# Optimization experiments

Hardware: AMD Instinct MI355X
Metric: run time of the kernel (lower is better)

## Reference

```python
import jax, jax.numpy as jnp
import numpy as np

EMBED_DIM = 1024
NUM_HEADS = 16
HEAD_DIM = EMBED_DIM // NUM_HEADS


def setup_inputs() -> dict:
    key = jax.random.key(0)
    k_x, k_wqkv, k_bqkv, k_wout, k_bout = jax.random.split(key, 5)
    B, T, C = 2, 2048, EMBED_DIM
    s = 1.0 / np.sqrt(C)
    return {
        "x": jax.random.normal(k_x, (B, T, C), dtype=jnp.float32),
        "W_qkv": jax.random.uniform(k_wqkv, (C, 3 * C), jnp.float32, -s, s),
        "b_qkv": jax.random.uniform(k_bqkv, (3 * C,), jnp.float32, -s, s),
        "W_out": jax.random.uniform(k_wout, (C, C), jnp.float32, -s, s),
        "b_out": jax.random.uniform(k_bout, (C,), jnp.float32, -s, s),
    }


def reference(x, W_qkv, b_qkv, W_out, b_out):
    B, T, C = x.shape
    H, D = NUM_HEADS, HEAD_DIM
    qkv = x @ W_qkv + b_qkv                      # [B,T,3C]
    # Faithful to torch: reshape to [B,T,H,3D], move heads, chunk last dim.
    qkv = qkv.reshape(B, T, H, 3 * D).transpose(0, 2, 1, 3)  # [B,H,T,3D]
    q, k, v = qkv[..., :D], qkv[..., D:2 * D], qkv[..., 2 * D:]
    scores = jnp.einsum("bhqd,bhkd->bhqk", q, k) / np.sqrt(D).astype(jnp.float32)
    weights = jax.nn.softmax(scores, axis=-1)    # [B,H,T,T]
    attn = jnp.einsum("bhqk,bhkd->bhqd", weights, v)  # [B,H,T,D]
    attn = attn.transpose(0, 2, 1, 3).reshape(B, T, C)
    return attn @ W_out + b_out
```

## Files before the change

### kernel.cpp

```cpp
#include <hip/hip_runtime.h>


typedef float  f32x4  __attribute__((ext_vector_type(4)));
typedef __bf16 bf16x8 __attribute__((ext_vector_type(8)));

#define QSCALE 0.18033688011112042f

#if __has_builtin(__builtin_amdgcn_exp2f)
#define EXP2(x) __builtin_amdgcn_exp2f(x)
#else
#define EXP2(x) exp2f(x)
#endif
#if __has_builtin(__builtin_amdgcn_rcpf)
#define RCP(x) __builtin_amdgcn_rcpf(x)
#else
#define RCP(x) (1.0f / (x))
#endif

static __device__ __forceinline__ f32x4 mfma32(bf16x8 a, bf16x8 b, f32x4 c) {
    return __builtin_amdgcn_mfma_f32_16x16x32_bf16(a, b, c, 0, 0, 0);
}

static __device__ __forceinline__ bf16x8 ld8(const unsigned short* p) {
    return __builtin_bit_cast(bf16x8, *(const uint4*)p);
}
static __device__ __forceinline__ unsigned short bfbits(float f) {
    __bf16 h = (__bf16)f;
    return __builtin_bit_cast(unsigned short, h);
}

static __device__ __forceinline__ void glds16(const unsigned short* g,
                                              unsigned short* lds_base) {
    __builtin_amdgcn_global_load_lds(
        (const __attribute__((address_space(1))) unsigned int*)g,
        (__attribute__((address_space(3))) unsigned int*)lds_base, 16, 0, 0);
}

__global__ __launch_bounds__(256) void prep_kernel(
    const float* __restrict__ x, unsigned short* __restrict__ xb,
    const float* __restrict__ Wqkv, unsigned short* __restrict__ wqkvT,
    const float* __restrict__ Wout, unsigned short* __restrict__ woutT) {
    __shared__ float tile[32][33];
    const int bid = blockIdx.x;
    if (bid < 4096) {
        int i = bid * 256 + threadIdx.x;
        float4 v = ((const float4*)x)[i];
        ushort4 o;
        o.x = bfbits(v.x); o.y = bfbits(v.y);
        o.z = bfbits(v.z); o.w = bfbits(v.w);
        ((ushort4*)xb)[i] = o;
        return;
    }
    const float* W; unsigned short* Wt; int N, n0, k0;
    if (bid < 7168) {
        int l = bid - 4096; W = Wqkv; Wt = wqkvT; N = 3072;
        n0 = (l % 96) * 32; k0 = (l / 96) * 32;
    } else {
        int l = bid - 7168; W = Wout; Wt = woutT; N = 1024;
        n0 = (l & 31) * 32; k0 = (l >> 5) * 32;
    }
    int tx = threadIdx.x & 31, ty = threadIdx.x >> 5;
#pragma unroll
    for (int i = 0; i < 4; i++) {
        int r = ty + i * 8;
        tile[r][tx] = W[(size_t)(k0 + r) * N + n0 + tx];
    }
    __syncthreads();
#pragma unroll
    for (int i = 0; i < 4; i++) {
        int r = ty + i * 8;
        Wt[(size_t)(n0 + r) * 1024 + k0 + tx] = bfbits(tile[tx][r]);
    }
}

__global__ __launch_bounds__(256) void qkv_gemm_kernel(
    const unsigned short* __restrict__ A, const unsigned short* __restrict__ Bt,
    const float* __restrict__ bias, unsigned short* __restrict__ Qb,
    unsigned short* __restrict__ Kb, unsigned short* __restrict__ Vtb) {
    __shared__ unsigned short As[2][128 * 32];
    __shared__ unsigned short Bs[2][128 * 32];
    const int wg = blockIdx.x;
    const int xcd = wg & 7, local = wg >> 3;
    const int n_t = (xcd >> 2) * 12 + local % 12;
    const int m_t = (xcd & 3) * 8 + local / 12;
    const int m0 = m_t * 128, n0 = n_t * 128;
    const int tid = threadIdx.x;
    const int lane = tid & 63, w = tid >> 6;
    const int ln = lane & 15, quad = lane >> 4;
    const int wm = (w >> 1) * 64, wn = (w & 1) * 64;
    const int sr = lane >> 2, sc = (lane & 3) * 8;
    f32x4 acc[4][4] = {};
#pragma unroll
    for (int i = 0; i < 2; i++) {
        int r0 = w * 32 + i * 16;
        glds16(&A[(size_t)(m0 + r0 + sr) * 1024 + sc], &As[0][r0 * 32]);
        glds16(&Bt[(size_t)(n0 + r0 + sr) * 1024 + sc], &Bs[0][r0 * 32]);
    }
    __syncthreads();
    for (int kt = 0; kt < 32; kt++) {
        const int cur = kt & 1;
        if (kt + 1 < 32) {
            const int nxt = cur ^ 1;
            const int kc = (kt + 1) * 32;
#pragma unroll
            for (int i = 0; i < 2; i++) {
                int r0 = w * 32 + i * 16;
                glds16(&A[(size_t)(m0 + r0 + sr) * 1024 + kc + sc], &As[nxt][r0 * 32]);
                glds16(&Bt[(size_t)(n0 + r0 + sr) * 1024 + kc + sc], &Bs[nxt][r0 * 32]);
            }
        }
        bf16x8 af[4], bf[4];
#pragma unroll
        for (int mi = 0; mi < 4; mi++)
            af[mi] = ld8(&As[cur][(wm + mi * 16 + ln) * 32 + quad * 8]);
#pragma unroll
        for (int ni = 0; ni < 4; ni++)
            bf[ni] = ld8(&Bs[cur][(wn + ni * 16 + ln) * 32 + quad * 8]);
#pragma unroll
        for (int mi = 0; mi < 4; mi++)
#pragma unroll
            for (int ni = 0; ni < 4; ni++)
                acc[mi][ni] = mfma32(af[mi], bf[ni], acc[mi][ni]);
        __syncthreads();
    }
#pragma unroll
    for (int mi = 0; mi < 4; mi++)
#pragma unroll
        for (int ni = 0; ni < 4; ni++) {
            int gn = n0 + wn + ni * 16 + ln;
            float bi = bias[gn];
            int h = gn / 192, rr = gn - h * 192;
            int gm0 = m0 + wm + mi * 16 + quad * 4;
            int b = gm0 >> 11, t0 = gm0 & 2047;
            float vv[4];
#pragma unroll
            for (int r = 0; r < 4; r++) vv[r] = acc[mi][ni][r] + bi;
            if (rr < 64) {
                size_t base = ((size_t)(b * 16 + h) * 2048 + t0) * 64 + rr;
#pragma unroll
                for (int r = 0; r < 4; r++)
                    Qb[base + (size_t)r * 64] = bfbits(vv[r] * QSCALE);
            } else if (rr < 128) {
                size_t base = ((size_t)(b * 16 + h) * 2048 + t0) * 64 + rr - 64;
#pragma unroll
                for (int r = 0; r < 4; r++)
                    Kb[base + (size_t)r * 64] = bfbits(vv[r]);
            } else {
                int tp0 = (t0 & ~31) | (quad << 3) | ((mi & 1) << 2);
                ushort4 pk;
                pk.x = bfbits(vv[0]); pk.y = bfbits(vv[1]);
                pk.z = bfbits(vv[2]); pk.w = bfbits(vv[3]);
                *(ushort4*)&Vtb[((size_t)(b * 16 + h) * 64 + (rr - 128)) * 2048
                                + tp0] = pk;
            }
        }
}

__global__ __launch_bounds__(512)
__attribute__((amdgpu_waves_per_eu(4, 4)))
void attn_kernel(
    const unsigned short* __restrict__ Q, const unsigned short* __restrict__ K,
    const unsigned short* __restrict__ Vt, unsigned short* __restrict__ Ob) {
    __shared__ unsigned short smem[2][2][2][4096];
    const int wg  = blockIdx.x;
    const int xcd = wg & 7, local = wg >> 3;
    const int bh  = xcd * 4 + (local >> 4);
    const int qt  = local & 15;
    const int tid = threadIdx.x;
    const int lane = tid & 63, w = tid >> 6;
    const int w4 = w & 3, ks = w >> 2;
    const int ln = lane & 15, quad = lane >> 4;
    const int lr = lane >> 3, lg = lane & 7;
    const int e = ln & 7;

    unsigned short (*Ks)[4096] = smem[ks][0];
    unsigned short (*Vs)[4096] = smem[ks][1];

    const unsigned short* Qg = Q + ((size_t)bh * 2048 + qt * 128) * 64;
    const unsigned short* Kg = K + ((size_t)bh * 2048 + ks * 1024) * 64;
    const unsigned short* Vg = Vt + (size_t)bh * 64 * 2048 + ks * 1024;

    bf16x8 qf[2][2];
#pragma unroll
    for (int h = 0; h < 2; h++) {
        const unsigned short* qp = Qg + (size_t)(w4 * 32 + h * 16 + ln) * 64;
        qf[h][0] = ld8(qp + quad * 8);
        qf[h][1] = ld8(qp + 32 + quad * 8);
    }

    const unsigned short* kb0 = &Ks[0][ln * 64 + (quad ^ e) * 8];
    const unsigned short* kb1 = &Ks[0][ln * 64 + ((4 + quad) ^ e) * 8];
    const unsigned short* vp0 = &Vs[0][ln * 64 + (quad ^ e) * 8];
    const unsigned short* vp1 = &Vs[0][ln * 64 + ((4 + quad) ^ e) * 8];

    const int kof0 = (w4 * 16 + lr) * 64 + (lg ^ lr) * 8;
    const int kof1 = (w4 * 16 + 8 + lr) * 64 + (lg ^ lr) * 8;
    const int vof0 = (w4 * 16 + lr) * 2048 + (lg ^ lr) * 8;
    const int vof1 = (w4 * 16 + 8 + lr) * 2048 + (lg ^ lr) * 8;
    unsigned short* kd0[2] = {&Ks[0][(w4 * 16) * 64], &Ks[1][(w4 * 16) * 64]};
    unsigned short* kd1[2] = {&Ks[0][(w4 * 16 + 8) * 64], &Ks[1][(w4 * 16 + 8) * 64]};
    unsigned short* vd0[2] = {&Vs[0][(w4 * 16) * 64], &Vs[1][(w4 * 16) * 64]};
    unsigned short* vd1[2] = {&Vs[0][(w4 * 16 + 8) * 64], &Vs[1][(w4 * 16 + 8) * 64]};

    glds16(Kg + kof0, kd0[0]);
    glds16(Kg + kof1, kd1[0]);
    glds16(Vg + vof0, vd0[0]);
    glds16(Vg + vof1, vd1[0]);
    __syncthreads();

    const unsigned short* KgR = Kg + 4096;
    const unsigned short* VgR = Vg + 64;

    bf16x8 ones8;
#pragma unroll
    for (int j = 0; j < 8; j++) ones8[j] = __bf16(1.0f);
    f32x4 zero4 = {};
    asm volatile("" : "+v"(zero4));
    f32x4 o[2][4] = {};
    f32x4 lacc[2] = {};

#define ATTN_TILE(CUR, PREF)                                                  \
    do {                                                                      \
        if (PREF) {                                                           \
            glds16(KgR + kof0, kd0[CUR ^ 1]);                                 \
            glds16(KgR + kof1, kd1[CUR ^ 1]);                                 \
            glds16(VgR + vof0, vd0[CUR ^ 1]);                                 \
            glds16(VgR + vof1, vd1[CUR ^ 1]);                                 \
            KgR += 4096; VgR += 64;                                           \
        }                                                                     \
        f32x4 s[2][4];                                                        \
        __builtin_amdgcn_s_setprio(1);                                        \
        _Pragma("unroll")                                                     \
        for (int ms = 0; ms < 4; ms++) {                                      \
            bf16x8 a0 = ld8(kb0 + (CUR) * 4096 + ms * 1024);                  \
            bf16x8 a1 = ld8(kb1 + (CUR) * 4096 + ms * 1024);                  \
            _Pragma("unroll")                                                 \
            for (int h = 0; h < 2; h++) {                                     \
                s[h][ms] = mfma32(a0, qf[h][0], zero4);                       \
                s[h][ms] = mfma32(a1, qf[h][1], s[h][ms]);                    \
            }                                                                 \
        }                                                                     \
        __builtin_amdgcn_s_setprio(0);                                        \
        bf16x8 pb8[2][2];                                                     \
        _Pragma("unroll")                                                     \
        for (int h = 0; h < 2; h++)                                           \
            _Pragma("unroll")                                                 \
            for (int p = 0; p < 2; p++) {                                     \
                f32x4 e0, e1;                                                 \
                e0[0] = EXP2(s[h][2 * p][0]); e0[1] = EXP2(s[h][2 * p][1]);   \
                e0[2] = EXP2(s[h][2 * p][2]); e0[3] = EXP2(s[h][2 * p][3]);   \
                e1[0] = EXP2(s[h][2 * p + 1][0]);                             \
                e1[1] = EXP2(s[h][2 * p + 1][1]);                             \
                e1[2] = EXP2(s[h][2 * p + 1][2]);                             \
                e1[3] = EXP2(s[h][2 * p + 1][3]);                             \
                pb8[h][p][0] = __bf16(e0[0]); pb8[h][p][1] = __bf16(e0[1]);   \
                pb8[h][p][2] = __bf16(e0[2]); pb8[h][p][3] = __bf16(e0[3]);   \
                pb8[h][p][4] = __bf16(e1[0]); pb8[h][p][5] = __bf16(e1[1]);   \
                pb8[h][p][6] = __bf16(e1[2]); pb8[h][p][7] = __bf16(e1[3]);   \
            }                                                                 \
        __builtin_amdgcn_s_setprio(1);                                        \
        _Pragma("unroll")                                                     \
        for (int h = 0; h < 2; h++)                                           \
            _Pragma("unroll")                                                 \
            for (int p = 0; p < 2; p++)                                       \
                lacc[h] = mfma32(ones8, pb8[h][p], lacc[h]);                  \
        _Pragma("unroll")                                                     \
        for (int df = 0; df < 4; df++) {                                      \
            bf16x8 a80 = ld8(vp0 + (CUR) * 4096 + df * 1024);                 \
            o[0][df] = mfma32(a80, pb8[0][0], o[0][df]);                      \
            o[1][df] = mfma32(a80, pb8[1][0], o[1][df]);                      \
            bf16x8 a81 = ld8(vp1 + (CUR) * 4096 + df * 1024);                 \
            o[0][df] = mfma32(a81, pb8[0][1], o[0][df]);                      \
            o[1][df] = mfma32(a81, pb8[1][1], o[1][df]);                      \
        }                                                                     \
        __builtin_amdgcn_s_setprio(0);                                        \
        __syncthreads();                                                      \
    } while (0)

    for (int it = 0; it < 8; it++) {
        ATTN_TILE(0, true);
        ATTN_TILE(1, (it < 7));
    }
#undef ATTN_TILE

    float* xf = (float*)&smem[0][0][0][0];
    const int slot = w4 * 64 + lane;
    if (ks) {
#pragma unroll
        for (int h = 0; h < 2; h++)
#pragma unroll
            for (int df = 0; df < 4; df++) {
                int j = h * 4 + df;
                *(f32x4*)(xf + (size_t)(slot * 8 + (j ^ (slot & 7))) * 4) = o[h][df];
            }
        xf[8192 + slot * 2 + 0] = lacc[0][0];
        xf[8192 + slot * 2 + 1] = lacc[1][0];
    }
    __syncthreads();
    if (!ks) {
        float inv0 = RCP(lacc[0][0] + xf[8192 + slot * 2 + 0]);
        float inv1 = RCP(lacc[1][0] + xf[8192 + slot * 2 + 1]);
        const int b = bh >> 4, hh = bh & 15;
#pragma unroll
        for (int h = 0; h < 2; h++) {
            float inv = h ? inv1 : inv0;
            int qrow = qt * 128 + w4 * 32 + h * 16 + ln;
            size_t row = ((size_t)b * 2048 + qrow) * 1024 + hh * 64;
#pragma unroll
            for (int df = 0; df < 4; df++) {
                int j = h * 4 + df;
                f32x4 oo = *(const f32x4*)(xf + (size_t)(slot * 8 + (j ^ (slot & 7))) * 4);
                ushort4 pk;
                pk.x = bfbits((o[h][df][0] + oo[0]) * inv);
                pk.y = bfbits((o[h][df][1] + oo[1]) * inv);
                pk.z = bfbits((o[h][df][2] + oo[2]) * inv);
                pk.w = bfbits((o[h][df][3] + oo[3]) * inv);
                *(ushort4*)&Ob[row + df * 16 + quad * 4] = pk;
            }
        }
    }
}

__global__ __launch_bounds__(256) void out_gemm_kernel(
    const unsigned short* __restrict__ A, const unsigned short* __restrict__ Bt,
    const float* __restrict__ bias, float* __restrict__ out) {
    __shared__ unsigned short As[2][64 * 32];
    __shared__ unsigned short Bs[2][128 * 32];
    const int wg = blockIdx.x;
    const int xcd = wg & 7, local = wg >> 3;
    const int m_t = xcd * 8 + (local & 7);
    const int n_t = local >> 3;
    const int m0 = m_t * 64, n0 = n_t * 128;
    const int tid = threadIdx.x;
    const int lane = tid & 63, w = tid >> 6;
    const int ln = lane & 15, quad = lane >> 4;
    const int wm = (w >> 1) * 32, wn = (w & 1) * 64;
    const int sr = lane >> 2, sc = (lane & 3) * 8;
    f32x4 acc[2][4] = {};
    {
        int ra = w * 16;
        glds16(&A[(size_t)(m0 + ra + sr) * 1024 + sc], &As[0][ra * 32]);
#pragma unroll
        for (int i = 0; i < 2; i++) {
            int rb = w * 32 + i * 16;
            glds16(&Bt[(size_t)(n0 + rb + sr) * 1024 + sc], &Bs[0][rb * 32]);
        }
    }
    __syncthreads();
    for (int kt = 0; kt < 32; kt++) {
        const int cur = kt & 1;
        if (kt + 1 < 32) {
            const int nxt = cur ^ 1;
            const int kc = (kt + 1) * 32;
            int ra = w * 16;
            glds16(&A[(size_t)(m0 + ra + sr) * 1024 + kc + sc], &As[nxt][ra * 32]);
#pragma unroll
            for (int i = 0; i < 2; i++) {
                int rb = w * 32 + i * 16;
                glds16(&Bt[(size_t)(n0 + rb + sr) * 1024 + kc + sc], &Bs[nxt][rb * 32]);
            }
        }
        bf16x8 af[2], bf[4];
#pragma unroll
        for (int mi = 0; mi < 2; mi++)
            af[mi] = ld8(&As[cur][(wm + mi * 16 + ln) * 32 + quad * 8]);
#pragma unroll
        for (int ni = 0; ni < 4; ni++)
            bf[ni] = ld8(&Bs[cur][(wn + ni * 16 + ln) * 32 + quad * 8]);
#pragma unroll
        for (int mi = 0; mi < 2; mi++)
#pragma unroll
            for (int ni = 0; ni < 4; ni++)
                acc[mi][ni] = mfma32(af[mi], bf[ni], acc[mi][ni]);
        __syncthreads();
    }
#pragma unroll
    for (int mi = 0; mi < 2; mi++)
#pragma unroll
        for (int ni = 0; ni < 4; ni++) {
            int gn = n0 + wn + ni * 16 + ln;
            float bi = bias[gn];
#pragma unroll
            for (int r = 0; r < 4; r++) {
                int gm = m0 + wm + mi * 16 + quad * 4 + r;
                out[(size_t)gm * 1024 + gn] = acc[mi][ni][r] + bi;
            }
        }
}

extern "C" void kernel_launch(void* const* d_in, const int* in_sizes, int n_in,
                              void* d_out, int out_size, void* d_ws, size_t ws_size,
                              hipStream_t stream) {
    const float* x     = (const float*)d_in[0];
    const float* W_qkv = (const float*)d_in[1];
    const float* b_qkv = (const float*)d_in[2];
    const float* W_out = (const float*)d_in[3];
    const float* b_out = (const float*)d_in[4];
    float* out = (float*)d_out;

    char* ws = (char*)d_ws;
    unsigned short* xb    = (unsigned short*)(ws);
    unsigned short* wqkvT = (unsigned short*)(ws + (size_t)( 8 << 20));
    unsigned short* woutT = (unsigned short*)(ws + (size_t)(14 << 20));
    unsigned short* Qb    = (unsigned short*)(ws + (size_t)(16 << 20));
    unsigned short* Kb    = (unsigned short*)(ws + (size_t)(24 << 20));
    unsigned short* Vtb   = (unsigned short*)(ws + (size_t)(32 << 20));
    unsigned short* attnb = (unsigned short*)(ws + (size_t)(40 << 20));

    prep_kernel<<<8192, 256, 0, stream>>>(x, xb, W_qkv, wqkvT, W_out, woutT);
    qkv_gemm_kernel<<<768, 256, 0, stream>>>(xb, wqkvT, b_qkv, Qb, Kb, Vtb);
    attn_kernel<<<512, 512, 0, stream>>>(Qb, Kb, Vtb, attnb);
    out_gemm_kernel<<<512, 256, 0, stream>>>(attnb, woutT, b_out, out);
}
```

Measured before the change: 177.0 us.

## Enlarge QKV GEMM tiles to 256x192 with 512 threads aligned to heads

The QKV projection GEMM goes from 128x128 tiles with 256 threads to 256x192 tiles with 512 threads (8 waves, each computing 64x96). Each N tile now matches one head's 192-column q/k/v slice, so the head index is simply the tile index and the per-element division is gone. The aim is more data reuse per LDS load and fewer workgroups (256 instead of 768), with the XCD mapping adjusted to match. The cost is more LDS and registers per block and only 256 blocks, which may under-fill the GPU's compute units.

```diff
diff --git a/kernel.cpp b/kernel.cpp
--- a/kernel.cpp
+++ b/kernel.cpp
@@ -73,63 +73,67 @@
     }
 }
 
-__global__ __launch_bounds__(256) void qkv_gemm_kernel(
+__global__ __launch_bounds__(512) void qkv_gemm_kernel(
     const unsigned short* __restrict__ A, const unsigned short* __restrict__ Bt,
     const float* __restrict__ bias, unsigned short* __restrict__ Qb,
     unsigned short* __restrict__ Kb, unsigned short* __restrict__ Vtb) {
-    __shared__ unsigned short As[2][128 * 32];
-    __shared__ unsigned short Bs[2][128 * 32];
+    __shared__ unsigned short As[2][256 * 32];
+    __shared__ unsigned short Bs[2][192 * 32];
     const int wg = blockIdx.x;
     const int xcd = wg & 7, local = wg >> 3;
-    const int n_t = (xcd >> 2) * 12 + local % 12;
-    const int m_t = (xcd & 3) * 8 + local / 12;
-    const int m0 = m_t * 128, n0 = n_t * 128;
+    const int n_t = (xcd & 3) * 4 + (local & 3);
+    const int m_t = (xcd >> 2) * 8 + (local >> 2);
+    const int m0 = m_t * 256, n0 = n_t * 192;
     const int tid = threadIdx.x;
     const int lane = tid & 63, w = tid >> 6;
     const int ln = lane & 15, quad = lane >> 4;
-    const int wm = (w >> 1) * 64, wn = (w & 1) * 64;
+    const int wm = (w >> 1) * 64;
+    const int wn = (w & 1) * 96;
     const int sr = lane >> 2, sc = (lane & 3) * 8;
-    f32x4 acc[4][4] = {};
-#pragma unroll
-    for (int i = 0; i < 2; i++) {
-        int r0 = w * 32 + i * 16;
-        glds16(&A[(size_t)(m0 + r0 + sr) * 1024 + sc], &As[0][r0 * 32]);
-        glds16(&Bt[(size_t)(n0 + r0 + sr) * 1024 + sc], &Bs[0][r0 * 32]);
-    }
+
+    f32x4 acc[4][6] = {};
+
+#define STAGE(BUF, KC)                                                        \
+    do {                                                                      \
+        glds16(&A[(size_t)(m0 + w * 16 + sr) * 1024 + (KC) + sc],             \
+               &As[BUF][(w * 16) * 32]);                                      \
+        glds16(&A[(size_t)(m0 + 128 + w * 16 + sr) * 1024 + (KC) + sc],       \
+               &As[BUF][(128 + w * 16) * 32]);                                \
+        glds16(&Bt[(size_t)(n0 + w * 16 + sr) * 1024 + (KC) + sc],            \
+               &Bs[BUF][(w * 16) * 32]);                                      \
+        if (w < 4)                                                            \
+            glds16(&Bt[(size_t)(n0 + 128 + w * 16 + sr) * 1024 + (KC) + sc],  \
+                   &Bs[BUF][(128 + w * 16) * 32]);                            \
+    } while (0)
+
+    STAGE(0, 0);
     __syncthreads();
     for (int kt = 0; kt < 32; kt++) {
         const int cur = kt & 1;
-        if (kt + 1 < 32) {
-            const int nxt = cur ^ 1;
-            const int kc = (kt + 1) * 32;
-#pragma unroll
-            for (int i = 0; i < 2; i++) {
-                int r0 = w * 32 + i * 16;
-                glds16(&A[(size_t)(m0 + r0 + sr) * 1024 + kc + sc], &As[nxt][r0 * 32]);
-                glds16(&Bt[(size_t)(n0 + r0 + sr) * 1024 + kc + sc], &Bs[nxt][r0 * 32]);
-            }
-        }
-        bf16x8 af[4], bf[4];
+        if (kt + 1 < 32) STAGE(cur ^ 1, (kt + 1) * 32);
+        bf16x8 af[4], bf[6];
 #pragma unroll
         for (int mi = 0; mi < 4; mi++)
             af[mi] = ld8(&As[cur][(wm + mi * 16 + ln) * 32 + quad * 8]);
 #pragma unroll
-        for (int ni = 0; ni < 4; ni++)
+        for (int ni = 0; ni < 6; ni++)
             bf[ni] = ld8(&Bs[cur][(wn + ni * 16 + ln) * 32 + quad * 8]);
 #pragma unroll
         for (int mi = 0; mi < 4; mi++)
 #pragma unroll
-            for (int ni = 0; ni < 4; ni++)
+            for (int ni = 0; ni < 6; ni++)
                 acc[mi][ni] = mfma32(af[mi], bf[ni], acc[mi][ni]);
         __syncthreads();
     }
+#undef STAGE
+
+    const int h = n_t;
 #pragma unroll
     for (int mi = 0; mi < 4; mi++)
 #pragma unroll
-        for (int ni = 0; ni < 4; ni++) {
-            int gn = n0 + wn + ni * 16 + ln;
-            float bi = bias[gn];
-            int h = gn / 192, rr = gn - h * 192;
+        for (int ni = 0; ni < 6; ni++) {
+            int rr = wn + ni * 16 + ln;
+            float bi = bias[n0 + rr];
             int gm0 = m0 + wm + mi * 16 + quad * 4;
             int b = gm0 >> 11, t0 = gm0 & 2047;
             float vv[4];
@@ -408,7 +412,7 @@
     unsigned short* attnb = (unsigned short*)(ws + (size_t)(40 << 20));
 
     prep_kernel<<<8192, 256, 0, stream>>>(x, xb, W_qkv, wqkvT, W_out, woutT);
-    qkv_gemm_kernel<<<768, 256, 0, stream>>>(xb, wqkvT, b_qkv, Qb, Kb, Vtb);
+    qkv_gemm_kernel<<<256, 512, 0, stream>>>(xb, wqkvT, b_qkv, Qb, Kb, Vtb);
     attn_kernel<<<512, 512, 0, stream>>>(Qb, Kb, Vtb, attnb);
     out_gemm_kernel<<<512, 256, 0, stream>>>(attnb, woutT, b_out, out);
 }
```

New measurement: 173.9 us. Within noise of the previous version (-1.8%).

## Triple-buffer QKV GEMM LDS staging with one barrier per k-step

Applied to the files above, without the earlier changes.

The QKV projection GEMM goes from double to triple-buffered LDS tiles. Global-to-LDS loads are issued two k-steps ahead, and the waits use explicit vmcnt counts with a single s_barrier per iteration instead of a full __syncthreads after compute. Address pointers are precomputed, and the MFMA block is wrapped in s_setprio to favour matrix issue. This aims to hide global load latency and cut barrier stalls, at the cost of extra LDS per block, which may reduce occupancy.

```diff
diff --git a/kernel.cpp b/kernel.cpp
--- a/kernel.cpp
+++ b/kernel.cpp
@@ -77,8 +77,8 @@
     const unsigned short* __restrict__ A, const unsigned short* __restrict__ Bt,
     const float* __restrict__ bias, unsigned short* __restrict__ Qb,
     unsigned short* __restrict__ Kb, unsigned short* __restrict__ Vtb) {
-    __shared__ unsigned short As[2][128 * 32];
-    __shared__ unsigned short Bs[2][128 * 32];
+    __shared__ unsigned short As[3][128 * 32];
+    __shared__ unsigned short Bs[3][128 * 32];
     const int wg = blockIdx.x;
     const int xcd = wg & 7, local = wg >> 3;
     const int n_t = (xcd >> 2) * 12 + local % 12;
@@ -89,40 +89,67 @@
     const int ln = lane & 15, quad = lane >> 4;
     const int wm = (w >> 1) * 64, wn = (w & 1) * 64;
     const int sr = lane >> 2, sc = (lane & 3) * 8;
+
+    const unsigned short* a_rd = &As[0][(wm + ln) * 32 + quad * 8];
+    const unsigned short* b_rd = &Bs[0][(wn + ln) * 32 + quad * 8];
+    unsigned short* a_st0 = &As[0][(w * 32) * 32];
+    unsigned short* a_st1 = &As[0][(w * 32 + 16) * 32];
+    unsigned short* b_st0 = &Bs[0][(w * 32) * 32];
+    unsigned short* b_st1 = &Bs[0][(w * 32 + 16) * 32];
+    const unsigned short* Ag0 = &A[(size_t)(m0 + w * 32 + sr) * 1024 + sc];
+    const unsigned short* Ag1 = &A[(size_t)(m0 + w * 32 + 16 + sr) * 1024 + sc];
+    const unsigned short* Bg0 = &Bt[(size_t)(n0 + w * 32 + sr) * 1024 + sc];
+    const unsigned short* Bg1 = &Bt[(size_t)(n0 + w * 32 + 16 + sr) * 1024 + sc];
+
+#define QSTAGE(OFF, KC)                                                       \
+    do {                                                                      \
+        glds16(Ag0 + (KC), a_st0 + (OFF));                                    \
+        glds16(Bg0 + (KC), b_st0 + (OFF));                                    \
+        glds16(Ag1 + (KC), a_st1 + (OFF));                                    \
+        glds16(Bg1 + (KC), b_st1 + (OFF));                                    \
+    } while (0)
+
+#define QCOMPUTE(CO)                                                          \
+    do {                                                                      \
+        bf16x8 af[4], bf[4];                                                  \
+        _Pragma("unroll")                                                     \
+        for (int mi = 0; mi < 4; mi++)                                        \
+            af[mi] = ld8(a_rd + (CO) + mi * 512);                             \
+        _Pragma("unroll")                                                     \
+        for (int ni = 0; ni < 4; ni++)                                        \
+            bf[ni] = ld8(b_rd + (CO) + ni * 512);                             \
+        __builtin_amdgcn_s_setprio(1);                                        \
+        _Pragma("unroll")                                                     \
+        for (int mi = 0; mi < 4; mi++)                                        \
+            _Pragma("unroll")                                                 \
+            for (int ni = 0; ni < 4; ni++)                                    \
+                acc[mi][ni] = mfma32(af[mi], bf[ni], acc[mi][ni]);            \
+        __builtin_amdgcn_s_setprio(0);                                        \
+    } while (0)
+
     f32x4 acc[4][4] = {};
-#pragma unroll
-    for (int i = 0; i < 2; i++) {
-        int r0 = w * 32 + i * 16;
-        glds16(&A[(size_t)(m0 + r0 + sr) * 1024 + sc], &As[0][r0 * 32]);
-        glds16(&Bt[(size_t)(n0 + r0 + sr) * 1024 + sc], &Bs[0][r0 * 32]);
-    }
-    __syncthreads();
-    for (int kt = 0; kt < 32; kt++) {
-        const int cur = kt & 1;
-        if (kt + 1 < 32) {
-            const int nxt = cur ^ 1;
-            const int kc = (kt + 1) * 32;
-#pragma unroll
-            for (int i = 0; i < 2; i++) {
-                int r0 = w * 32 + i * 16;
-                glds16(&A[(size_t)(m0 + r0 + sr) * 1024 + kc + sc], &As[nxt][r0 * 32]);
-                glds16(&Bt[(size_t)(n0 + r0 + sr) * 1024 + kc + sc], &Bs[nxt][r0 * 32]);
-            }
-        }
-        bf16x8 af[4], bf[4];
-#pragma unroll
-        for (int mi = 0; mi < 4; mi++)
-            af[mi] = ld8(&As[cur][(wm + mi * 16 + ln) * 32 + quad * 8]);
-#pragma unroll
-        for (int ni = 0; ni < 4; ni++)
-            bf[ni] = ld8(&Bs[cur][(wn + ni * 16 + ln) * 32 + quad * 8]);
-#pragma unroll
-        for (int mi = 0; mi < 4; mi++)
-#pragma unroll
-            for (int ni = 0; ni < 4; ni++)
-                acc[mi][ni] = mfma32(af[mi], bf[ni], acc[mi][ni]);
-        __syncthreads();
-    }
+    QSTAGE(0, 0);
+    QSTAGE(4096, 32);
+    int co = 0;
+    int so = 2 * 4096;
+    for (int kt = 0; kt < 31; kt++) {
+        asm volatile("s_waitcnt vmcnt(4)" ::: "memory");
+        __builtin_amdgcn_sched_barrier(0);
+        asm volatile("s_barrier" ::: "memory");
+        __builtin_amdgcn_sched_barrier(0);
+        if (kt + 2 < 32) QSTAGE(so, (kt + 2) * 32);
+        QCOMPUTE(co);
+        co = (co == 2 * 4096) ? 0 : co + 4096;
+        so = (so == 2 * 4096) ? 0 : so + 4096;
+    }
+    asm volatile("s_waitcnt vmcnt(0)" ::: "memory");
+    __builtin_amdgcn_sched_barrier(0);
+    asm volatile("s_barrier" ::: "memory");
+    __builtin_amdgcn_sched_barrier(0);
+    QCOMPUTE(co);
+#undef QSTAGE
+#undef QCOMPUTE
+
 #pragma unroll
     for (int mi = 0; mi < 4; mi++)
 #pragma unroll
```

Result: faster. 171.6 us (-3.1%).
